# Kernel optimization log

Hardware: AMD Instinct MI355X
Metric: run time of the kernel (lower is better)

The kernel has to match this reference:

```python
import jax, jax.numpy as jnp
import numpy as np

B, CIN, COUT, H, W = 2, 256, 256, 96, 96
K, PAD, G = 3, 1, 4           # kernel, padding, deformable_groups
KK = K * K
CG = CIN // G                 # channels per deformable group


def setup_inputs() -> dict:
    key = jax.random.key(0)
    k1, k2, k3, k4 = jax.random.split(key, 4)
    feature = jax.random.normal(k1, (B, CIN, H, W), jnp.float32)
    pred_shape = jax.random.normal(k2, (B, H * W, 4), jnp.float32)
    # init_weights: normal(std=0.01), no biases
    w_offset = jax.random.normal(k3, (G * KK * 2, 4, 1, 1), jnp.float32) * 0.01
    w_deform = jax.random.normal(k4, (COUT, CIN, K, K), jnp.float32) * 0.01
    return {"feature": feature, "pred_shape": pred_shape,
            "w_offset": w_offset, "w_deform": w_deform}


def reference(feature, pred_shape, w_offset, w_deform):
    # pred_shape: (B, H*W, 4) -> (B, 4, H, W); detached in the original
    ps = jnp.transpose(pred_shape, (0, 2, 1)).reshape(B, -1, H, W)
    ps = jax.lax.stop_gradient(ps)
    # 1x1 offset conv: (B, G*2*KK, H, W)
    offset = jnp.einsum('bchw,oc->bohw', ps, w_offset[:, :, 0, 0])
    # mmcv layout per group: [y_k0, x_k0, y_k1, x_k1, ...]
    off = offset.reshape(B, G, KK, 2, H, W)
    off_y, off_x = off[:, :, :, 0], off[:, :, :, 1]   # (B, G, KK, H, W)

    kk = jnp.arange(KK)
    ky = (kk // K).reshape(KK, 1, 1).astype(jnp.float32)
    kx = (kk % K).reshape(KK, 1, 1).astype(jnp.float32)
    yy = jnp.arange(H, dtype=jnp.float32).reshape(1, H, 1)
    xx = jnp.arange(W, dtype=jnp.float32).reshape(1, 1, W)
    # sampling positions (stride=1, dilation=1): (B, G, KK, H, W)
    py = (yy - PAD + ky)[None, None] + off_y
    px = (xx - PAD + kx)[None, None] + off_x

    img = feature.reshape(B, G, CG, H * W)

    def gather(yi, xi):
        # zero outside the image (matches DCN bilinear with zero padding)
        valid = ((yi >= 0) & (yi < H) & (xi >= 0) & (xi < W)).astype(feature.dtype)
        idx = jnp.clip(yi, 0, H - 1) * W + jnp.clip(xi, 0, W - 1)
        v = jnp.take_along_axis(img, idx.reshape(B, G, 1, KK * H * W), axis=3)
        return v.reshape(B, G, CG, KK, H, W) * valid[:, :, None]

    y0 = jnp.floor(py); x0 = jnp.floor(px)
    ly = py - y0; lx = px - x0
    y0i = y0.astype(jnp.int32); x0i = x0.astype(jnp.int32)

    val = ((1 - ly) * (1 - lx))[:, :, None] * gather(y0i, x0i) \
        + ((1 - ly) * lx)[:, :, None] * gather(y0i, x0i + 1) \
        + (ly * (1 - lx))[:, :, None] * gather(y0i + 1, x0i) \
        + (ly * lx)[:, :, None] * gather(y0i + 1, x0i + 1)

    sampled = val.reshape(B, CIN, KK, H, W)
    out = jnp.einsum('bckhw,ock->bohw', sampled, w_deform.reshape(COUT, CIN, KK))
    return jax.nn.relu(out)
```

## Files before the change

kernel.cpp:

```cpp
#include <hip/hip_runtime.h>
#include <hip/hip_bf16.h>
#include <stdint.h>

#define HH   96
#define WW   96
#define HW   9216
#define CIN  256
#define COUT 256
#define NB   2
#define NG   4
#define CG   64
#define KK   9
#define KTOT 2304
#define KB   288
#define TS   8
#define WIN  12
#define SCH  32

typedef __attribute__((ext_vector_type(8))) short short8;
typedef __attribute__((ext_vector_type(4))) float f32x4;
typedef __attribute__((ext_vector_type(4))) uint32_t u32x4;

__device__ __forceinline__ uint32_t pk2bf(float v0, float v1) {
    __hip_bfloat162 h = __float22bfloat162_rn(make_float2(v0, v1));
    uint32_t u;
    __builtin_memcpy(&u, &h, 4);
    return u;
}

__global__ __launch_bounds__(256) void prep_A(const float* __restrict__ wd,
                                              uint16_t* __restrict__ Ablk) {
    int t  = blockIdx.x * 256 + threadIdx.x;
    int kb = t % KB;
    int o  = t / KB;
    int kkA = kb >> 5;
    int c0A = (kb & 31) * 8;
    const float* src = wd + (size_t)o * KTOT + c0A * KK + kkA;
    float a[8];
#pragma unroll
    for (int e = 0; e < 8; ++e) a[e] = src[e * KK];
    uint16_t* dst = Ablk + ((size_t)kb * 256 + o) * 8;
    u32x4 v;
    v.x = pk2bf(a[0], a[1]);
    v.y = pk2bf(a[2], a[3]);
    v.z = pk2bf(a[4], a[5]);
    v.w = pk2bf(a[6], a[7]);
    *(u32x4*)dst = v;
}

__global__ __launch_bounds__(256) void sampler(const float* __restrict__ feature,
                                               const float* __restrict__ pred,
                                               const float* __restrict__ woff,
                                               uint16_t* __restrict__ S) {
    __shared__ float ft[SCH * WIN * WIN];

    int tid = threadIdx.x;
    int cb = blockIdx.y, b = blockIdx.z;
    int ch0 = cb * SCH;
    int g = ch0 >> 6;
    int ty = blockIdx.x / (WW / TS), tx = blockIdx.x % (WW / TS);
    int r0 = ty * TS, c0 = tx * TS;
    int rlo = min(max(r0 - 2, 0), HH - WIN);
    int clo = min(max(c0 - 2, 0), WW - WIN);

    const float* fg = feature + ((size_t)(b * CIN + ch0)) * HW;
    for (int e = tid; e < SCH * WIN * WIN; e += 256) {
        int ch = e / (WIN * WIN);
        int re = e - ch * (WIN * WIN);
        int rr = re / WIN, cc = re - rr * WIN;
        ft[e] = fg[(size_t)ch * HW + (rlo + rr) * WW + clo + cc];
    }
    __syncthreads();

    int lane = tid & 63, wv = tid >> 6;
    int lr = lane >> 3, lc = lane & 7;
    int hy = r0 + lr, hx = c0 + lc;
    int p = hy * WW + hx;
    float4 ps4 = *(const float4*)(pred + ((size_t)b * HW + p) * 4);

    const float* ftw = ft + (wv * 8) * (WIN * WIN);
    const float* fgw = fg + (size_t)(wv * 8) * HW;
    int kb_base = cb * 4 + wv;

#pragma unroll
    for (int kk = 0; kk < KK; ++kk) {
        const float* wy = woff + (g * KK + kk) * 8;
        float offy = ps4.x * wy[0] + ps4.y * wy[1] + ps4.z * wy[2] + ps4.w * wy[3];
        float offx = ps4.x * wy[4] + ps4.y * wy[5] + ps4.z * wy[6] + ps4.w * wy[7];
        float py = (float)(hy - 1 + kk / 3) + offy;
        float px = (float)(hx - 1 + kk % 3) + offx;
        float fy = floorf(py), fx = floorf(px);
        int y0 = (int)fy, x0 = (int)fx;
        float ly = py - fy, lx = px - fx;
        int r = min(max(y0, 0), HH - 2);
        int q = min(max(x0, 0), WW - 2);
        float wyA = (y0 == r) ? (1.f - ly) : ((y0 == -1) ? ly : 0.f);
        float wyB = (y0 == r) ? ly : ((y0 == HH - 1) ? (1.f - ly) : 0.f);
        float wxA = (x0 == q) ? (1.f - lx) : ((x0 == -1) ? lx : 0.f);
        float wxB = (x0 == q) ? lx : ((x0 == WW - 1) ? (1.f - lx) : 0.f);
        float c00 = wyA * wxA, c01 = wyA * wxB;
        float c10 = wyB * wxA, c11 = wyB * wxB;

        bool fast = (r >= rlo) & (r <= rlo + WIN - 2) &
                    (q >= clo) & (q <= clo + WIN - 2);

        uint16_t* Sp = S + (((size_t)b * KB + (kk * 32 + kb_base)) * HW + p) * 8;
        uint32_t pk[4];

        if (fast) {
            int base = (r - rlo) * WIN + (q - clo);
#pragma unroll
            for (int ep = 0; ep < 4; ++ep) {
                const float* f0 = ftw + (2 * ep) * (WIN * WIN) + base;
                const float* f1 = f0 + (WIN * WIN);
                float v0 = c00 * f0[0] + c01 * f0[1] + c10 * f0[WIN] + c11 * f0[WIN + 1];
                float v1 = c00 * f1[0] + c01 * f1[1] + c10 * f1[WIN] + c11 * f1[WIN + 1];
                pk[ep] = pk2bf(v0, v1);
            }
        } else {
            size_t gb = (size_t)r * WW + q;
#pragma unroll
            for (int ep = 0; ep < 4; ++ep) {
                const float* f0 = fgw + (size_t)(2 * ep) * HW + gb;
                const float* f1 = f0 + HW;
                float v0 = c00 * f0[0] + c01 * f0[1] + c10 * f0[WW] + c11 * f0[WW + 1];
                float v1 = c00 * f1[0] + c01 * f1[1] + c10 * f1[WW] + c11 * f1[WW + 1];
                pk[ep] = pk2bf(v0, v1);
            }
        }
        u32x4 vv = {pk[0], pk[1], pk[2], pk[3]};
        *(u32x4*)(Sp) = vv;
    }
}

__global__ __launch_bounds__(256) void gemm_kernel(const uint16_t* __restrict__ S,
                                                   const uint16_t* __restrict__ Ablk,
                                                   float* __restrict__ out) {
    __shared__ uint16_t sA[2][8 * 64 * 8];
    __shared__ uint16_t sB[2][8 * 64 * 8];

    int tid = threadIdx.x;
    int lane = tid & 63, wv = tid >> 6;
    int wr = wv >> 1, wc = wv & 1;
    int col0 = blockIdx.x * 64;
    int o0   = blockIdx.y * 64;
    int b    = blockIdx.z;

    const uint16_t* Bg = S + (size_t)b * KB * HW * 8;

    f32x4 acc[2][2];
#pragma unroll
    for (int m = 0; m < 2; ++m)
#pragma unroll
        for (int n = 0; n < 2; ++n) acc[m][n] = (f32x4){0.f, 0.f, 0.f, 0.f};

    int kc = lane >> 4, il = lane & 15;
    const int NT = KTOT / 64;

    auto STAGE = [&](int t, int buf) {
#pragma unroll
        for (int j = 0; j < 2; ++j) {
            int kb = t * 8 + wv * 2 + j;
            int lc_ = wv * 2 + j;
            __builtin_amdgcn_global_load_lds(
                (const __attribute__((address_space(1))) uint32_t*)
                    (Ablk + ((size_t)kb * 256 + o0 + lane) * 8),
                (__attribute__((address_space(3))) uint32_t*)
                    (&sA[buf][(lc_ * 64 + lane) * 8]),
                16, 0, 0);
            __builtin_amdgcn_global_load_lds(
                (const __attribute__((address_space(1))) uint32_t*)
                    (Bg + ((size_t)kb * HW + col0 + lane) * 8),
                (__attribute__((address_space(3))) uint32_t*)
                    (&sB[buf][(lc_ * 64 + lane) * 8]),
                16, 0, 0);
        }
    };

    STAGE(0, 0);
    STAGE(1, 1);

    for (int t = 0; t < NT; ++t) {
        int cur = t & 1;
        if (t < NT - 1) {
            asm volatile("s_waitcnt vmcnt(4)\n\ts_barrier" ::: "memory");
        } else {
            asm volatile("s_waitcnt vmcnt(0)\n\ts_barrier" ::: "memory");
        }
        __builtin_amdgcn_sched_barrier(0);

        short8 af[2][2], bf[2][2];
#pragma unroll
        for (int h = 0; h < 2; ++h) {
#pragma unroll
            for (int m = 0; m < 2; ++m)
                af[h][m] = *(const short8*)(&sA[cur][((h * 4 + kc) * 64 + wr * 32 + m * 16 + il) * 8]);
#pragma unroll
            for (int n = 0; n < 2; ++n)
                bf[h][n] = *(const short8*)(&sB[cur][((h * 4 + kc) * 64 + wc * 32 + n * 16 + il) * 8]);
        }

#pragma unroll
        for (int h = 0; h < 2; ++h)
#pragma unroll
            for (int m = 0; m < 2; ++m)
#pragma unroll
                for (int n = 0; n < 2; ++n)
                    acc[m][n] = __builtin_amdgcn_mfma_f32_16x16x32_bf16(af[h][m], bf[h][n], acc[m][n], 0, 0, 0);

        asm volatile("s_waitcnt lgkmcnt(0)\n\ts_barrier" ::: "memory");
        __builtin_amdgcn_sched_barrier(0);
        if (t + 2 < NT) STAGE(t + 2, cur);
    }

    int r4 = (lane >> 4) * 4;
    size_t obase = ((size_t)b * COUT + o0 + wr * 32) * HW + col0 + wc * 32;
#pragma unroll
    for (int m = 0; m < 2; ++m)
#pragma unroll
        for (int n = 0; n < 2; ++n)
#pragma unroll
            for (int r = 0; r < 4; ++r) {
                float v = acc[m][n][r];
                v = v > 0.f ? v : 0.f;
                out[obase + (size_t)(m * 16 + r4 + r) * HW + n * 16 + il] = v;
            }
}

extern "C" void kernel_launch(void* const* d_in, const int* in_sizes, int n_in,
                              void* d_out, int out_size, void* d_ws, size_t ws_size,
                              hipStream_t stream) {
    (void)in_sizes; (void)n_in; (void)out_size; (void)ws_size;
    const float* feature = (const float*)d_in[0];
    const float* pred    = (const float*)d_in[1];
    const float* woff    = (const float*)d_in[2];
    const float* wdef    = (const float*)d_in[3];
    float* out = (float*)d_out;

    const size_t S_BYTES = (size_t)NB * KB * HW * 8 * 2;
    uint16_t* S    = (uint16_t*)d_ws;
    uint16_t* Ablk = (uint16_t*)((char*)d_ws + S_BYTES);

    hipLaunchKernelGGL(prep_A, dim3(288), dim3(256), 0, stream, wdef, Ablk);
    hipLaunchKernelGGL(sampler, dim3((HH / TS) * (WW / TS), CIN / SCH, NB), dim3(256), 0, stream,
                       feature, pred, woff, S);
    hipLaunchKernelGGL(gemm_kernel, dim3(HW / 64, COUT / 64, NB), dim3(256), 0, stream,
                       S, Ablk, out);
}
```

Before: 93.72 us.

## Load GEMM A fragments directly to registers and double output-channel tile

The GEMM block tile grows from 64 to 128 output channels, so each wave computes a 64x32 tile with 8 accumulators and half as many blocks are launched. A-operand weight fragments are no longer staged through LDS; each wave loads them straight from global memory into registers, double-buffered one k-step ahead, while B keeps the LDS path. The intent is to reuse each staged B tile across more output channels and cut LDS traffic for A. In exchange it raises register pressure (launch bounds set to 3 blocks), has wave pairs that share rows load the same A data redundantly from global, and halves grid parallelism.

```diff
diff --git a/kernel.cpp b/kernel.cpp
--- a/kernel.cpp
+++ b/kernel.cpp
@@ -133,41 +133,44 @@
     }
 }
 
-__global__ __launch_bounds__(256) void gemm_kernel(const uint16_t* __restrict__ S,
-                                                   const uint16_t* __restrict__ Ablk,
-                                                   float* __restrict__ out) {
-    __shared__ uint16_t sA[2][8 * 64 * 8];
+__global__ __launch_bounds__(256, 3) void gemm_kernel(const uint16_t* __restrict__ S,
+                                                      const uint16_t* __restrict__ Ablk,
+                                                      float* __restrict__ out) {
     __shared__ uint16_t sB[2][8 * 64 * 8];
 
     int tid = threadIdx.x;
     int lane = tid & 63, wv = tid >> 6;
     int wr = wv >> 1, wc = wv & 1;
     int col0 = blockIdx.x * 64;
-    int o0   = blockIdx.y * 64;
+    int o0   = blockIdx.y * 128;
     int b    = blockIdx.z;
 
     const uint16_t* Bg = S + (size_t)b * KB * HW * 8;
 
-    f32x4 acc[2][2];
-#pragma unroll
-    for (int m = 0; m < 2; ++m)
+    f32x4 acc[4][2];
+#pragma unroll
+    for (int m = 0; m < 4; ++m)
 #pragma unroll
         for (int n = 0; n < 2; ++n) acc[m][n] = (f32x4){0.f, 0.f, 0.f, 0.f};
 
     int kc = lane >> 4, il = lane & 15;
     const int NT = KTOT / 64;
 
-    auto STAGE = [&](int t, int buf) {
+    const uint16_t* Arow = Ablk + ((size_t)(o0 + wr * 64 + il)) * 8;
+
+    auto LOADA = [&](int t, short8 (&af)[2][4]) {
+#pragma unroll
+        for (int h = 0; h < 2; ++h)
+#pragma unroll
+            for (int m = 0; m < 4; ++m)
+                af[h][m] = *(const short8*)(Arow + ((size_t)(t * 8 + h * 4 + kc) * 256 + m * 16) * 8);
+    };
+
+    auto STAGEB = [&](int t, int buf) {
 #pragma unroll
         for (int j = 0; j < 2; ++j) {
             int kb = t * 8 + wv * 2 + j;
             int lc_ = wv * 2 + j;
-            __builtin_amdgcn_global_load_lds(
-                (const __attribute__((address_space(1))) uint32_t*)
-                    (Ablk + ((size_t)kb * 256 + o0 + lane) * 8),
-                (__attribute__((address_space(3))) uint32_t*)
-                    (&sA[buf][(lc_ * 64 + lane) * 8]),
-                16, 0, 0);
             __builtin_amdgcn_global_load_lds(
                 (const __attribute__((address_space(1))) uint32_t*)
                     (Bg + ((size_t)kb * HW + col0 + lane) * 8),
@@ -177,46 +180,51 @@
         }
     };
 
-    STAGE(0, 0);
-    STAGE(1, 1);
-
-    for (int t = 0; t < NT; ++t) {
-        int cur = t & 1;
+    short8 afA[2][4], afB[2][4];
+
+    LOADA(0, afA);
+    STAGEB(0, 0);
+    STAGEB(1, 1);
+
+    auto ITER = [&](int t, short8 (&use)[2][4], short8 (&next)[2][4], int buf) {
         if (t < NT - 1) {
-            asm volatile("s_waitcnt vmcnt(4)\n\ts_barrier" ::: "memory");
+            asm volatile("s_waitcnt vmcnt(2)\n\ts_barrier" ::: "memory");
         } else {
             asm volatile("s_waitcnt vmcnt(0)\n\ts_barrier" ::: "memory");
         }
         __builtin_amdgcn_sched_barrier(0);
 
-        short8 af[2][2], bf[2][2];
-#pragma unroll
-        for (int h = 0; h < 2; ++h) {
-#pragma unroll
-            for (int m = 0; m < 2; ++m)
-                af[h][m] = *(const short8*)(&sA[cur][((h * 4 + kc) * 64 + wr * 32 + m * 16 + il) * 8]);
+        if (t + 1 < NT) LOADA(t + 1, next);
+
+        short8 bf[2][2];
+#pragma unroll
+        for (int h = 0; h < 2; ++h)
 #pragma unroll
             for (int n = 0; n < 2; ++n)
-                bf[h][n] = *(const short8*)(&sB[cur][((h * 4 + kc) * 64 + wc * 32 + n * 16 + il) * 8]);
-        }
+                bf[h][n] = *(const short8*)(&sB[buf][((h * 4 + kc) * 64 + wc * 32 + n * 16 + il) * 8]);
 
 #pragma unroll
         for (int h = 0; h < 2; ++h)
 #pragma unroll
-            for (int m = 0; m < 2; ++m)
+            for (int m = 0; m < 4; ++m)
 #pragma unroll
                 for (int n = 0; n < 2; ++n)
-                    acc[m][n] = __builtin_amdgcn_mfma_f32_16x16x32_bf16(af[h][m], bf[h][n], acc[m][n], 0, 0, 0);
+                    acc[m][n] = __builtin_amdgcn_mfma_f32_16x16x32_bf16(use[h][m], bf[h][n], acc[m][n], 0, 0, 0);
 
         asm volatile("s_waitcnt lgkmcnt(0)\n\ts_barrier" ::: "memory");
         __builtin_amdgcn_sched_barrier(0);
-        if (t + 2 < NT) STAGE(t + 2, cur);
+        if (t + 2 < NT) STAGEB(t + 2, buf);
+    };
+
+    for (int tt = 0; tt < NT; tt += 2) {
+        ITER(tt,     afA, afB, 0);
+        ITER(tt + 1, afB, afA, 1);
     }
 
     int r4 = (lane >> 4) * 4;
-    size_t obase = ((size_t)b * COUT + o0 + wr * 32) * HW + col0 + wc * 32;
-#pragma unroll
-    for (int m = 0; m < 2; ++m)
+    size_t obase = ((size_t)b * COUT + o0 + wr * 64) * HW + col0 + wc * 32;
+#pragma unroll
+    for (int m = 0; m < 4; ++m)
 #pragma unroll
         for (int n = 0; n < 2; ++n)
 #pragma unroll
@@ -244,6 +252,6 @@
     hipLaunchKernelGGL(prep_A, dim3(288), dim3(256), 0, stream, wdef, Ablk);
     hipLaunchKernelGGL(sampler, dim3((HH / TS) * (WW / TS), CIN / SCH, NB), dim3(256), 0, stream,
                        feature, pred, woff, S);
-    hipLaunchKernelGGL(gemm_kernel, dim3(HW / 64, COUT / 64, NB), dim3(256), 0, stream,
+    hipLaunchKernelGGL(gemm_kernel, dim3(HW / 64, COUT / 128, NB), dim3(256), 0, stream,
                        S, Ablk, out);
 }
```

Result: faster. 86.92 us (-7.3%).
